# Kernel optimization log

Hardware: AMD Instinct MI355X
Metric: run time of the kernel (lower is better)

## Reference

```python
import jax, jax.numpy as jnp
import numpy as np

# ---- static physical configuration (matches init_kwargs param dict) ----
NX = NY = 513
NL = 3
N_ENS = 4
LX = LY = 5120.0e3
DX = LX / (NX - 1)
DY = LY / (NY - 1)
F0 = 9.375e-5
BETA = 1.754e-11
A2 = 0.0
A4 = 2.0e9
DELTA_EK = 2.0
TAU0 = 2.0e-5
BCCO = 0.2
ZFBC = BCCO / (1.0 + 0.5 * BCCO)
DT = 600.0
NUM_STEPS = 4
HEIGHTS = np.array([350.0, 750.0, 2900.0])
RED_G = np.array([0.025, 0.0125])

JAC_COEF = 1.0 / (F0 * DX * DY)
HYPERDIFF_COEF = A4 / F0**2 / DX**6
BOTTOM_FRICTION_COEF = DELTA_EK / (2.0 * abs(F0) * DX**2 * (-HEIGHTS[-1]))


def _build_constants():
    """Precompute stratification / mode / Helmholtz matrices (float64 numpy, cast to f32)."""
    A = np.zeros((NL, NL))
    A[0, 0] = 1.0 / (HEIGHTS[0] * RED_G[0])
    A[0, 1] = -1.0 / (HEIGHTS[0] * RED_G[0])
    for i in range(1, NL - 1):
        A[i, i - 1] = -1.0 / (HEIGHTS[i] * RED_G[i - 1])
        A[i, i] = 1.0 / HEIGHTS[i] * (1.0 / RED_G[i] + 1.0 / RED_G[i - 1])
        A[i, i + 1] = -1.0 / (HEIGHTS[i] * RED_G[i])
    A[-1, -1] = 1.0 / (HEIGHTS[NL - 1] * RED_G[NL - 2])
    A[-1, -2] = -1.0 / (HEIGHTS[NL - 1] * RED_G[NL - 2])
    lam_r, R = np.linalg.eig(A)
    lam_l, L = np.linalg.eig(A.T)
    lam_r, R, lam_l, L = lam_r.real, R.real, lam_l.real, L.real
    # align left eigenvectors with right eigenvalue ordering (biorthogonality)
    order = np.array([int(np.argmin(np.abs(lam_l - lr))) for lr in lam_r])
    L = L[:, order]
    Cl2m = np.diag(1.0 / np.diag(L.T @ R)) @ L.T
    Cm2l = R
    lambd = lam_r
    # DST-I eigenvalues of the 5-point Laplacian on the interior grid
    xg, yg = np.meshgrid(np.arange(1, NX - 1), np.arange(1, NY - 1), indexing='ij')
    lap_dst = (2 * (np.cos(np.pi / (NX - 1) * xg) - 1) / DX**2
               + 2 * (np.cos(np.pi / (NY - 1) * yg) - 1) / DY**2)
    helm_dst = lap_dst[None] / F0**2 - lambd[:, None, None]  # (nl, nx-2, ny-2)

    def np_dstI1D(x):
        N = x.shape[-1]
        xp = np.zeros(x.shape[:-1] + (N + 2,))
        xp[..., 1:-1] = x
        return np.fft.irfft(-1j * xp, n=2 * (N + 1), axis=-1, norm='ortho')[..., 1:N + 1]

    def np_dstI2D(x):
        return np.swapaxes(np_dstI1D(np.swapaxes(np_dstI1D(x), -1, -2)), -1, -2)

    const = np.ones((NL, NX, NY)) / (NX * NY)
    s = np.zeros_like(const)
    s[:, 1:-1, 1:-1] = np_dstI2D(np_dstI2D(const[:, 1:-1, 1:-1]) / helm_dst)
    hom_sol = (const + s * lambd[:, None, None])[:-1]  # (nl-1, nx, ny)
    M = (Cm2l[1:] - Cm2l[:-1])[:NL - 1, :NL - 1] * hom_sol.mean((1, 2))[None, :]
    alpha = -np.linalg.inv(M) @ (Cm2l[1:, :-1] - Cm2l[:-1, :-1])
    # wind forcing: curl(tau)/(f0*H1) on interior points; tau_y = 0, tau_x(y) only
    tau_x = -TAU0 * np.cos(2 * np.pi * (np.arange(NY) + 0.5) / NY)[None, :] * np.ones((NX, NY))
    dtaux_dy = (tau_x[1:-1, 2:] - tau_x[1:-1, :-2]) / (2 * DY)
    wind = (-dtaux_dy / (F0 * HEIGHTS[0]))[None]  # (1, nx-2, ny-2)
    f32 = lambda a: jnp.asarray(a, jnp.float32)
    return dict(A=f32(A), Cl2m=f32(Cl2m), Cm2l=f32(Cm2l), helmoltz_dst=f32(helm_dst),
                alpha_matrix=f32(alpha), homogeneous_sol=f32(hom_sol), wind_forcing=f32(wind))


# ---------------- stencil ops ----------------

def _pad11(x):
    return jnp.pad(x, [(0, 0)] * (x.ndim - 2) + [(1, 1), (1, 1)])


def laplacian_h_nobc(f):
    # unscaled 5-point Laplacian, interior values only: (..., nx-2, ny-2)
    return (f[..., 2:, 1:-1] + f[..., :-2, 1:-1] + f[..., 1:-1, 2:] + f[..., 1:-1, :-2]
            - 4.0 * f[..., 1:-1, 1:-1])


def laplacian_h(f, fc):
    # full-grid Laplacian with partial-slip boundary treatment (coefficient fc = zfbc)
    lap = _pad11(laplacian_h_nobc(f))
    lap = lap.at[..., 0, :].set(fc * (f[..., 1, :] - f[..., 0, :]))
    lap = lap.at[..., -1, :].set(fc * (f[..., -2, :] - f[..., -1, :]))
    lap = lap.at[..., :, 0].set(fc * (f[..., :, 1] - f[..., :, 0]))
    lap = lap.at[..., :, -1].set(fc * (f[..., :, -2] - f[..., :, -1]))
    return lap


def laplacian_h_boundaries(f, fc):
    # boundary Laplacian values, concat order: x=0 (y interior), x=-1, y=0 (full x), y=-1
    return jnp.concatenate([
        fc * (f[..., 1, 1:-1] - f[..., 0, 1:-1]),
        fc * (f[..., -2, 1:-1] - f[..., -1, 1:-1]),
        fc * (f[..., :, 1] - f[..., :, 0]),
        fc * (f[..., :, -2] - f[..., :, -1])], axis=-1)


def jacobi_h(f, g):
    # Arakawa 9-point Jacobian J(f, g), interior values (..., nx-2, ny-2)
    dx_f = f[..., 2:, :] - f[..., :-2, :]
    dx_g = g[..., 2:, :] - g[..., :-2, :]
    dy_f = f[..., 2:] - f[..., :-2]
    dy_g = g[..., 2:] - g[..., :-2]
    return ((dx_f[..., 1:-1] * dy_g[..., 1:-1, :] - dx_g[..., 1:-1] * dy_f[..., 1:-1, :])
            + (f[..., 2:, 1:-1] * dy_g[..., 2:, :] - f[..., :-2, 1:-1] * dy_g[..., :-2, :])
            - (f[..., 1:-1, 2:] * dx_g[..., 2:] - f[..., 1:-1, :-2] * dx_g[..., :-2])
            + (g[..., 1:-1, 2:] * dx_f[..., 2:] - g[..., 1:-1, :-2] * dx_f[..., :-2])
            - (g[..., 2:, 1:-1] * dy_f[..., 2:, :] - g[..., :-2, 1:-1] * dy_f[..., :-2, :])) / 12.0


# ---------------- DST-I elliptic solve ----------------

def dstI1D(x):
    N = x.shape[-1]
    z = jnp.zeros(x.shape[:-1] + (1,), x.dtype)
    xp = jnp.concatenate([z, x, z], axis=-1)
    return jnp.fft.irfft(-1j * xp.astype(jnp.complex64), n=2 * (N + 1), axis=-1,
                         norm='ortho')[..., 1:N + 1]


def dstI2D(x):
    return jnp.swapaxes(dstI1D(jnp.swapaxes(dstI1D(x), -1, -2)), -1, -2)


def inverse_elliptic_dst(f, op_dst):
    return dstI2D(dstI2D(f) / op_dst)


# ---------------- QG time derivative ----------------

def _time_derivatives(y, A, Cl2m, Cm2l, helm_dst, alpha, hom_sol, wind):
    q, p = y[0], y[1]  # (..., nl, nx, ny)
    # advection + hyperdiffusion RHS on interior (a_2 == 0 branch skipped as in source)
    rhs = JAC_COEF * jacobi_h(q, p)
    delta2_p = laplacian_h(p, ZFBC)
    rhs = rhs - HYPERDIFF_COEF * laplacian_h_nobc(laplacian_h(delta2_p, ZFBC))
    rhs = rhs.at[..., 0:1, :, :].add(wind)
    rhs = rhs.at[..., -1:, :, :].add(BOTTOM_FRICTION_COEF * laplacian_h_nobc(p[..., -1:, :, :]))
    dq = _pad11(rhs)
    # layers -> modes, DST Helmholtz inversion, homogeneous-solution correction
    rhs_h = jnp.einsum('ij,...jxy->...ixy', Cl2m, dq)
    dp_modes = _pad11(inverse_elliptic_dst(rhs_h[..., 1:-1, 1:-1], helm_dst))
    mean_m = dp_modes[..., :-1, :, :].mean((-2, -1))  # (..., nl-1)
    dalpha = jnp.einsum('ij,...j->...i', alpha, mean_m)[..., None, None]
    dp_modes = dp_modes.at[..., :-1, :, :].add(dalpha * hom_sol)
    dp = jnp.einsum('ij,...jxy->...ixy', Cm2l, dp_modes)
    # boundary vorticity update
    dp_bound = jnp.concatenate([dp[..., 0, 1:-1], dp[..., -1, 1:-1],
                                dp[..., :, 0], dp[..., :, -1]], axis=-1)
    delta_p_bound = laplacian_h_boundaries(dp / (F0 * DX)**2, ZFBC)
    dq_bound = delta_p_bound - jnp.einsum('ij,...jl->...il', A, dp_bound)
    ny2 = NY - 2
    dq = dq.at[..., 0, 1:-1].set(dq_bound[..., :ny2])
    dq = dq.at[..., -1, 1:-1].set(dq_bound[..., ny2:2 * ny2])
    dq = dq.at[..., :, 0].set(dq_bound[..., 2 * ny2:2 * ny2 + NX])
    dq = dq.at[..., :, -1].set(dq_bound[..., 2 * ny2 + NX:2 * ny2 + 2 * NX])
    return jnp.stack((dq, dp), 0)


def _forecast(y0, t, A, Cl2m, Cm2l, helm_dst, alpha, hom_sol, wind):
    deriv = lambda y: _time_derivatives(y, A, Cl2m, Cm2l, helm_dst, alpha, hom_sol, wind)

    def step(y, dt_):
        k1 = deriv(y)
        k2 = deriv(y + 0.5 * dt_ * k1)
        k3 = deriv(y + 0.5 * dt_ * k2)
        k4 = deriv(y + dt_ * k3)
        y_next = y + (dt_ / 6.0) * (k1 + 2.0 * k2 + 2.0 * k3 + k4)
        return y_next, y_next

    _, traj = jax.lax.scan(step, y0, t[1:] - t[:-1])
    return jnp.concatenate([y0[None], traj], axis=0)  # (T, 2, n_ens, nl, nx, ny)


def setup_inputs() -> dict:
    key = jax.random.key(0)
    y0 = 0.1 * jax.random.normal(key, (2, N_ENS, NL, NX, NY), dtype=jnp.float32)
    t = jnp.arange(NUM_STEPS + 1, dtype=jnp.float32) * DT
    consts = _build_constants()
    return dict(y0=y0, t=t, **consts)


def reference(y0, t, A, Cl2m, Cm2l, helmoltz_dst, alpha_matrix, homogeneous_sol, wind_forcing):
    return _forecast(y0, t, A, Cl2m, Cm2l, helmoltz_dst, alpha_matrix,
                     homogeneous_sol, wind_forcing)
```

## Files before the change

kernel.cpp:

```cpp
#include <hip/hip_runtime.h>
#include <math.h>

#define NXY 513
#define NIN 511
#define NL3 3
#define NE4 4
#define NB 12
#define GLD 512

static constexpr long FS  = (long)NE4 * NL3 * NXY * NXY;
static constexpr long GSZ = (long)NB * GLD * GLD;
static constexpr int  NSTEPS = 4;

static constexpr double dF0 = 9.375e-05;
static constexpr double dDX = 10000.0;
static constexpr float ZFBCf     = (float)(0.2 / (1.0 + 0.5 * 0.2));
static constexpr float JACCf     = (float)(1.0 / (dF0 * dDX * dDX));
static constexpr float HYPCf     = (float)(2.0e9 / (dF0 * dF0) / (dDX*dDX*dDX*dDX*dDX*dDX));
static constexpr float BFCf      = (float)(2.0 / (2.0 * dF0 * dDX * dDX * (-2900.0)));
static constexpr float INVF0DX2f = (float)(1.0 / ((dF0 * dDX) * (dF0 * dDX)));

typedef short  bf16x8 __attribute__((ext_vector_type(8)));
typedef float  f32x4  __attribute__((ext_vector_type(4)));
typedef unsigned int u32;
typedef __attribute__((address_space(1))) const u32 GAS;
typedef __attribute__((address_space(3))) u32 LAS;
#define GLDS(gp, lp) __builtin_amdgcn_global_load_lds((GAS*)(gp), (LAS*)(lp), 16, 0, 0)

__device__ __forceinline__ unsigned short f2bf(float x) {
    unsigned int u = __float_as_uint(x);
    return (unsigned short)((u + 0x7FFFu + ((u >> 16) & 1u)) >> 16);
}
__device__ __forceinline__ float bf2f(unsigned short h) {
    return __uint_as_float(((unsigned int)h) << 16);
}

__global__ void initB_kernel(unsigned short* __restrict__ BoH, unsigned short* __restrict__ BoL,
                             unsigned short* __restrict__ BeH, unsigned short* __restrict__ BeL) {
    int j = threadIdx.x;
    int n = blockIdx.x;
    int idx = n * 256 + j;
    int mo = ((n + 1) * (2 * j + 1)) & 1023;
    int me = ((n + 1) * (2 * j + 2)) & 1023;
    float fo = (float)(0.0625 * sin(M_PI * (double)mo / 512.0));
    float fe = (float)(0.0625 * sin(M_PI * (double)me / 512.0));
    unsigned short oh = f2bf(fo);
    BoH[idx] = oh; BoL[idx] = f2bf(fo - bf2f(oh));
    unsigned short eh = f2bf(fe);
    BeH[idx] = eh; BeL[idx] = f2bf(fe - bf2f(eh));
}

__global__ __launch_bounds__(256) void fused_rhs(
    float* __restrict__ kq, const float* __restrict__ q, const float* __restrict__ p,
    const float* __restrict__ wind)
{
    __shared__ float ps[22][72];
    __shared__ float qs[22][72];
    __shared__ float l1[22][72];
    __shared__ float l2[22][72];
    const int c  = blockIdx.z;
    const int x0 = 1 + blockIdx.y * 16;
    const int y0 = 1 + blockIdx.x * 64;
    const int t  = threadIdx.x;
    const size_t off = (size_t)c * NXY * NXY;
    const float* pp = p + off;
    const float* qp = q + off;

    for (int idx = t; idx < 22 * 70; idx += 256) {
        int i = idx / 70, j = idx % 70;
        int gx = x0 - 3 + i, gy = y0 - 3 + j;
        bool in = (gx >= 0 && gx < NXY && gy >= 0 && gy < NXY);
        size_t go = (size_t)gx * NXY + gy;
        ps[i][j] = in ? pp[go] : 0.f;
        qs[i][j] = in ? qp[go] : 0.f;
    }
    __syncthreads();

#define LAPBC(a, i, j, gx, gy) \
    ((gy) == 0       ? ZFBCf * (a[i][(j)+1] - a[i][j]) : \
     (gy) == NXY-1   ? ZFBCf * (a[i][(j)-1] - a[i][j]) : \
     (gx) == 0       ? ZFBCf * (a[(i)+1][j] - a[i][j]) : \
     (gx) == NXY-1   ? ZFBCf * (a[(i)-1][j] - a[i][j]) : \
     a[(i)+1][j] + a[(i)-1][j] + a[i][(j)+1] + a[i][(j)-1] - 4.f * a[i][j])

    for (int idx = t; idx < 20 * 68; idx += 256) {
        int i = 1 + idx / 68, j = 1 + idx % 68;
        int gx = x0 - 3 + i, gy = y0 - 3 + j;
        float v = 0.f;
        if (gx >= 0 && gx < NXY && gy >= 0 && gy < NXY) v = LAPBC(ps, i, j, gx, gy);
        l1[i][j] = v;
    }
    __syncthreads();

    for (int idx = t; idx < 18 * 66; idx += 256) {
        int i = 2 + idx / 66, j = 2 + idx % 66;
        int gx = x0 - 3 + i, gy = y0 - 3 + j;
        float v = 0.f;
        if (gx >= 0 && gx < NXY && gy >= 0 && gy < NXY) v = LAPBC(l1, i, j, gx, gy);
        l2[i][j] = v;
    }
    __syncthreads();
#undef LAPBC

    const int l = c % NL3;
    for (int idx = t; idx < 16 * 64; idx += 256) {
        int i = 3 + idx / 64, j = 3 + idx % 64;
        int gx = x0 - 3 + i, gy = y0 - 3 + j;
        if (gx > NIN || gy > NIN) continue;
        float fmm=qs[i-1][j-1], fm0=qs[i-1][j], fmp=qs[i-1][j+1];
        float f0m=qs[i][j-1],                    f0p=qs[i][j+1];
        float fpm=qs[i+1][j-1], fp0=qs[i+1][j], fpp=qs[i+1][j+1];
        float gmm=ps[i-1][j-1], gm0=ps[i-1][j], gmp=ps[i-1][j+1];
        float g0m=ps[i][j-1],   g00=ps[i][j],   g0p=ps[i][j+1];
        float gpm=ps[i+1][j-1], gp0=ps[i+1][j], gpp=ps[i+1][j+1];
        float J1 = (fp0 - fm0) * (g0p - g0m) - (gp0 - gm0) * (f0p - f0m);
        float J2 = fp0 * (gpp - gpm) - fm0 * (gmp - gmm);
        float J3 = f0p * (gpp - gmp) - f0m * (gpm - gmm);
        float J4 = g0p * (fpp - fmp) - g0m * (fpm - fmm);
        float J5 = gp0 * (fpp - fpm) - gm0 * (fmp - fmm);
        float jac = (J1 + J2 - J3 + J4 - J5) * (1.0f / 12.0f);
        float lap3 = l2[i+1][j] + l2[i-1][j] + l2[i][j+1] + l2[i][j-1] - 4.f * l2[i][j];
        float v = JACCf * jac - HYPCf * lap3;
        if (l == 0)       v += wind[(size_t)(gx-1) * NIN + (gy-1)];
        if (l == NL3-1)   v += BFCf * (gp0 + gm0 + g0p + g0m - 4.f * g00);
        kq[off + (size_t)gx * NXY + gy] = v;
    }
}

__global__ void l2m_kernel(unsigned short* __restrict__ Gh, unsigned short* __restrict__ Gl,
                           const float* __restrict__ kq, const float* __restrict__ Cl2m) {
    int p  = blockIdx.x * blockDim.x + threadIdx.x;
    int rx = blockIdx.y * blockDim.y + threadIdx.y;
    int e = blockIdx.z;
    int ry0 = 2 * p, ry1 = 2 * p + 1;
    float vA[3] = {0.f, 0.f, 0.f}, vB[3] = {0.f, 0.f, 0.f};
    if (rx < NIN) {
        size_t base = ((size_t)(e * NL3) * NXY + (rx + 1)) * NXY;
        if (ry0 < NIN) {
            float f0 = kq[base + ry0 + 1];
            float f1 = kq[base + (size_t)NXY*NXY + ry0 + 1];
            float f2 = kq[base + 2*(size_t)NXY*NXY + ry0 + 1];
            vA[0] = Cl2m[0]*f0 + Cl2m[1]*f1 + Cl2m[2]*f2;
            vA[1] = Cl2m[3]*f0 + Cl2m[4]*f1 + Cl2m[5]*f2;
            vA[2] = Cl2m[6]*f0 + Cl2m[7]*f1 + Cl2m[8]*f2;
        }
        if (ry1 < NIN) {
            float f0 = kq[base + ry1 + 1];
            float f1 = kq[base + (size_t)NXY*NXY + ry1 + 1];
            float f2 = kq[base + 2*(size_t)NXY*NXY + ry1 + 1];
            vB[0] = Cl2m[0]*f0 + Cl2m[1]*f1 + Cl2m[2]*f2;
            vB[1] = Cl2m[3]*f0 + Cl2m[4]*f1 + Cl2m[5]*f2;
            vB[2] = Cl2m[6]*f0 + Cl2m[7]*f1 + Cl2m[8]*f2;
        }
    }
#pragma unroll
    for (int i = 0; i < 3; ++i) {
        size_t pb = (size_t)(e * NL3 + i) * 262144;
        size_t po = pb + (size_t)rx * 256 + p;
        size_t pe = po + 131072;
        unsigned short ha = f2bf(vA[i]);
        Gh[po] = ha; Gl[po] = f2bf(vA[i] - bf2f(ha));
        unsigned short hb = f2bf(vB[i]);
        Gh[pe] = hb; Gl[pe] = f2bf(vB[i] - bf2f(hb));
    }
}

#define EPLD 68
__global__ __launch_bounds__(256, 3) void gemm_dst(
    const unsigned short* __restrict__ Ah, const unsigned short* __restrict__ Al,
    const unsigned short* __restrict__ BoH, const unsigned short* __restrict__ BoL,
    const unsigned short* __restrict__ BeH, const unsigned short* __restrict__ BeL,
    unsigned short* __restrict__ Ch, unsigned short* __restrict__ Cl,
    float* __restrict__ Cf, const float* __restrict__ helm, float* __restrict__ part)
{
    __shared__ __attribute__((aligned(16))) char lds[49152];
    __shared__ float red[256];
    float* ep1 = (float*)lds;
    float* ep2 = ep1 + 32 * EPLD;
    const int id = blockIdx.x;
    const int nblk = id / 96, rr = id - nblk * 96;
    const int b = rr >> 3, mblk = rr & 7;
    const int m0 = mblk << 6;
    const int n0t = nblk << 5;
    const int t = threadIdx.x;
    const int w = t >> 6, lane = t & 63;
    const int wn = w >> 1, wm = w & 1;
    const int lr = lane & 15, g = lane >> 4;
    const unsigned short* AbH = Ah + (size_t)b * 262144;
    const unsigned short* AbL = Al + (size_t)b * 262144;

    const int srA = t >> 2;
    const int scA = ((t & 3) ^ ((srA >> 1) & 3)) * 8;
    const size_t gA = (size_t)(m0 + srA) * 256 + scA;
    const int dA = t * 16;
    const int hid = t & 127;
    const int srB = hid >> 2;
    const int scB = ((hid & 3) ^ ((srB >> 1) & 3)) * 8;
    const size_t gB = (size_t)(n0t + srB) * 256 + scB;
    const unsigned short* B1 = (t < 128) ? BoH : BoL;
    const unsigned short* B2 = (t < 128) ? BeH : BeL;
    const int dB1 = ((t < 128) ? 16384 : 18432) + hid * 16;
    const int dB2 = ((t < 128) ? 20480 : 22528) + hid * 16;

    auto STAGE = [&](int buf, int kt) {
        char* bb = lds + buf * 24576;
        int ke = kt * 32;
        GLDS(AbH + gA + ke,          bb + dA);
        GLDS(AbL + gA + ke,          bb + 4096  + dA);
        GLDS(AbH + 131072 + gA + ke, bb + 8192  + dA);
        GLDS(AbL + 131072 + gA + ke, bb + 12288 + dA);
        GLDS(B1 + gB + ke, bb + dB1);
        GLDS(B2 + gB + ke, bb + dB2);
    };

    f32x4 accO[2] = {}, accE[2] = {};
    int abyte[2];
#pragma unroll
    for (int i = 0; i < 2; ++i) {
        int ar = wm*32 + i*16 + lr;
        abyte[i] = ar*64 + ((g ^ ((ar >> 1) & 3)) * 16);
    }
    const int brl = wn*16 + lr;
    const int bby = brl*64 + ((g ^ ((brl >> 1) & 3)) * 16);

    STAGE(0, 0);
    __syncthreads();
    for (int it = 0; it < 8; ++it) {
        const int buf = it & 1;
        if (it < 7) STAGE(buf ^ 1, it + 1);
        const char* bb = lds + buf * 24576;
        bf16x8 boH = *(const bf16x8*)(bb + 16384 + bby);
        bf16x8 boL = *(const bf16x8*)(bb + 18432 + bby);
        bf16x8 beH = *(const bf16x8*)(bb + 20480 + bby);
        bf16x8 beL = *(const bf16x8*)(bb + 22528 + bby);
#pragma unroll
        for (int i = 0; i < 2; ++i) {
            bf16x8 aoH = *(const bf16x8*)(bb + abyte[i]);
            bf16x8 aoL = *(const bf16x8*)(bb + 4096  + abyte[i]);
            bf16x8 aeH = *(const bf16x8*)(bb + 8192  + abyte[i]);
            bf16x8 aeL = *(const bf16x8*)(bb + 12288 + abyte[i]);
            accO[i] = __builtin_amdgcn_mfma_f32_16x16x32_bf16(aoH, boH, accO[i], 0, 0, 0);
            accO[i] = __builtin_amdgcn_mfma_f32_16x16x32_bf16(aoH, boL, accO[i], 0, 0, 0);
            accO[i] = __builtin_amdgcn_mfma_f32_16x16x32_bf16(aoL, boH, accO[i], 0, 0, 0);
            accE[i] = __builtin_amdgcn_mfma_f32_16x16x32_bf16(aeH, beH, accE[i], 0, 0, 0);
            accE[i] = __builtin_amdgcn_mfma_f32_16x16x32_bf16(aeH, beL, accE[i], 0, 0, 0);
            accE[i] = __builtin_amdgcn_mfma_f32_16x16x32_bf16(aeL, beH, accE[i], 0, 0, 0);
        }
        __syncthreads();
    }

    const int mode = b % NL3;
    const float* hp = helm ? (helm + (size_t)mode * NIN * NIN) : nullptr;
    const int nl = wn*16 + lr;
    const int r1g = n0t + nl;
    const int r2g = 510 - n0t - nl;
#pragma unroll
    for (int i = 0; i < 2; ++i) {
        int ml = wm*32 + i*16 + 4*g;
#pragma unroll
        for (int r = 0; r < 4; ++r) {
            float o = accO[i][r], e = accE[i][r];
            float v1 = o + e, v2 = o - e;
            int mg = m0 + ml + r;
            if (hp && mg < NIN) {
                v1 /= hp[(size_t)r1g * NIN + mg];
                v2 /= hp[(size_t)r2g * NIN + mg];
            }
            ep1[nl*EPLD + ml + r] = v1;
            ep2[nl*EPLD + ml + r] = v2;
        }
    }
    __syncthreads();

    float lsum = 0.f;
    {
        const int row = t >> 3;
        const int cb = (t & 7) * 8;
        const int r1 = n0t + row;
        const int r2 = 510 - n0t - row;
        float v1[8], v2[8];
#pragma unroll
        for (int k = 0; k < 8; ++k) { v1[k] = ep1[row*EPLD + cb + k]; v2[k] = ep2[row*EPLD + cb + k]; }
        if (Cf) {
            size_t c1 = (size_t)b*262144 + (size_t)r1*512 + m0 + cb;
            size_t c2 = (size_t)b*262144 + (size_t)r2*512 + m0 + cb;
            f32x4 a0 = {v1[0], v1[1], v1[2], v1[3]};
            f32x4 a1 = {v1[4], v1[5], v1[6], v1[7]};
            f32x4 b0 = {v2[0], v2[1], v2[2], v2[3]};
            f32x4 b1 = {v2[4], v2[5], v2[6], v2[7]};
            *(f32x4*)(Cf + c1) = a0; *(f32x4*)(Cf + c1 + 4) = a1;
            *(f32x4*)(Cf + c2) = b0; *(f32x4*)(Cf + c2 + 4) = b1;
            if (nblk == 0 && t < 64) Cf[(size_t)b*262144 + (size_t)511*512 + m0 + t] = 0.f;
#pragma unroll
            for (int k = 0; k < 8; ++k) lsum += v1[k];
            if (r1 != 255) {
#pragma unroll
                for (int k = 0; k < 8; ++k) lsum += v2[k];
            }
        } else {
            auto STROW = [&](int rrow, const float* v) {
                size_t po = (size_t)b*262144 + (size_t)rrow*256 + ((m0 + cb) >> 1);
                size_t pe = po + 131072;
                unsigned short eh[4], el[4], oh[4], ol[4];
#pragma unroll
                for (int k = 0; k < 4; ++k) {
                    float ve = v[2*k], vo = v[2*k+1];
                    eh[k] = f2bf(ve); el[k] = f2bf(ve - bf2f(eh[k]));
                    oh[k] = f2bf(vo); ol[k] = f2bf(vo - bf2f(oh[k]));
                }
                *(uint2*)(Ch + po) = make_uint2((u32)eh[0] | ((u32)eh[1] << 16), (u32)eh[2] | ((u32)eh[3] << 16));
                *(uint2*)(Cl + po) = make_uint2((u32)el[0] | ((u32)el[1] << 16), (u32)el[2] | ((u32)el[3] << 16));
                *(uint2*)(Ch + pe) = make_uint2((u32)oh[0] | ((u32)oh[1] << 16), (u32)oh[2] | ((u32)oh[3] << 16));
                *(uint2*)(Cl + pe) = make_uint2((u32)ol[0] | ((u32)ol[1] << 16), (u32)ol[2] | ((u32)ol[3] << 16));
            };
            STROW(r1, v1);
            STROW(r2, v2);
            if (nblk == 0 && t < 32) {
                size_t z = (size_t)b*262144 + (size_t)511*256 + (m0 >> 1) + t;
                Ch[z] = 0; Cl[z] = 0; Ch[z + 131072] = 0; Cl[z + 131072] = 0;
            }
        }
    }

    if (part && Cf && mode < 2) {
        __syncthreads();
        red[t] = lsum;
        __syncthreads();
        for (int w2 = 128; w2 >= 1; w2 >>= 1) {
            if (t < w2) red[t] += red[t + w2];
            __syncthreads();
        }
        if (t == 0) {
            int plane8 = (b / NL3) * 2 + mode;
            part[plane8 * 64 + nblk * 8 + mblk] = red[0];
        }
    }
}

__global__ __launch_bounds__(256) void m2l_bound(
    float* __restrict__ kp, float* __restrict__ kq,
    const float* __restrict__ G, const float* __restrict__ hom,
    const float* __restrict__ Cm2l, const float* __restrict__ Amat,
    const float* __restrict__ alpha, const float* __restrict__ part)
{
    __shared__ float sp[128];
    __shared__ float sdal[2];
    const int yy = blockIdx.x * 64 + threadIdx.x;
    const int xx = blockIdx.y * 4 + threadIdx.y;
    const int e  = blockIdx.z;
    const int tt = threadIdx.y * 64 + threadIdx.x;

    if (tt < 128) sp[tt] = part[(e*2 + (tt >> 6))*64 + (tt & 63)];
    __syncthreads();
    if (tt == 0) {
        float s0 = 0.f, s1 = 0.f;
        for (int j = 0; j < 64; ++j) { s0 += sp[j]; s1 += sp[64 + j]; }
        const float inv = 1.0f / ((float)NXY * (float)NXY);
        float mm0 = s0 * inv, mm1 = s1 * inv;
        sdal[0] = alpha[0]*mm0 + alpha[1]*mm1;
        sdal[1] = alpha[2]*mm0 + alpha[3]*mm1;
    }
    __syncthreads();
    if (xx >= NXY || yy >= NXY) return;
    const float dal0 = sdal[0], dal1 = sdal[1];

    auto DP = [&](int px, int py, float* dp) {
        bool inter = (px >= 1 && px <= NIN && py >= 1 && py <= NIN);
        float mv0 = 0.f, mv1 = 0.f, mv2 = 0.f;
        if (inter) {
            size_t gb = (size_t)(e*NL3)*GLD*GLD + (size_t)(px-1)*GLD + (py-1);
            mv0 = G[gb]; mv1 = G[gb + (size_t)GLD*GLD]; mv2 = G[gb + 2*(size_t)GLD*GLD];
        }
        mv0 += dal0 * hom[(size_t)px*NXY + py];
        mv1 += dal1 * hom[(size_t)NXY*NXY + (size_t)px*NXY + py];
        dp[0] = Cm2l[0]*mv0 + Cm2l[1]*mv1 + Cm2l[2]*mv2;
        dp[1] = Cm2l[3]*mv0 + Cm2l[4]*mv1 + Cm2l[5]*mv2;
        dp[2] = Cm2l[6]*mv0 + Cm2l[7]*mv1 + Cm2l[8]*mv2;
    };

    float dp[3];
    DP(xx, yy, dp);
#pragma unroll
    for (int l = 0; l < 3; ++l)
        kp[((size_t)(e*NL3 + l)*NXY + xx)*NXY + yy] = dp[l];

    const bool bnd = (xx == 0 || xx == NXY-1 || yy == 0 || yy == NXY-1);
    if (bnd) {
        int xn, yn;
        if      (yy == 0)      { xn = xx;    yn = 1; }
        else if (yy == NXY-1)  { xn = xx;    yn = NXY-2; }
        else if (xx == 0)      { xn = 1;     yn = yy; }
        else                   { xn = NXY-2; yn = yy; }
        float dpn[3];
        DP(xn, yn, dpn);
#pragma unroll
        for (int l = 0; l < 3; ++l) {
            float lpb = ZFBCf * INVF0DX2f * (dpn[l] - dp[l]);
            kq[((size_t)(e*NL3 + l)*NXY + xx)*NXY + yy] =
                lpb - (Amat[l*3+0]*dp[0] + Amat[l*3+1]*dp[1] + Amat[l*3+2]*dp[2]);
        }
    }
}

__global__ void rk_fused(float4* __restrict__ o1, float4* __restrict__ o2,
                         const float4* __restrict__ x, const float4* __restrict__ k,
                         float c1, float c2, int accumulate,
                         const float* __restrict__ t, int s, long n4) {
    float dt = t[s+1] - t[s];
    float a1 = c1 * dt, a2 = c2 * dt;
    for (long i = (long)blockIdx.x * blockDim.x + threadIdx.x; i < n4;
         i += (long)gridDim.x * blockDim.x) {
        float4 kk = k[i], xx = x[i];
        float4 b0 = accumulate ? o1[i] : xx;
        o1[i] = make_float4(b0.x + a1*kk.x, b0.y + a1*kk.y, b0.z + a1*kk.z, b0.w + a1*kk.w);
        if (o2) o2[i] = make_float4(xx.x + a2*kk.x, xx.y + a2*kk.y, xx.z + a2*kk.z, xx.w + a2*kk.w);
    }
}

__global__ void copy_kernel(float4* __restrict__ out, const float4* __restrict__ in, long n4) {
    for (long i = (long)blockIdx.x * blockDim.x + threadIdx.x; i < n4;
         i += (long)gridDim.x * blockDim.x)
        out[i] = in[i];
}

extern "C" void kernel_launch(void* const* d_in, const int* in_sizes, int n_in,
                              void* d_out, int out_size, void* d_ws, size_t ws_size,
                              hipStream_t stream) {
    const float* y0    = (const float*)d_in[0];
    const float* tarr  = (const float*)d_in[1];
    const float* Amat  = (const float*)d_in[2];
    const float* Cl2m  = (const float*)d_in[3];
    const float* Cm2l  = (const float*)d_in[4];
    const float* helm  = (const float*)d_in[5];
    const float* alpha = (const float*)d_in[6];
    const float* hom   = (const float*)d_in[7];
    const float* wind  = (const float*)d_in[8];
    float* out = (float*)d_out;
    char* base = (char*)d_ws;

    unsigned short* BoH = (unsigned short*)base;
    unsigned short* BoL = BoH + 65536;
    unsigned short* BeH = BoL + 65536;
    unsigned short* BeL = BeH + 65536;
    float* ytmp = (float*)(base + 1024*1024);
    float* kbuf = ytmp + 2*FS;
    char*  REGb = (char*)(kbuf + 2*FS);
    unsigned short* P0h = (unsigned short*)REGb;
    unsigned short* P0l = P0h + GSZ;
    unsigned short* P1h = P0l + GSZ;
    unsigned short* P1l = P1h + GSZ;
    float* R4 = (float*)REGb;
    float* partial = (float*)(REGb + (size_t)2*FS*sizeof(float));

    const dim3 bSt(64, 4, 1);
    const dim3 gSt4((NXY + 63)/64, (NXY + 3)/4, NE4);
    const dim3 gL2M(4, 128, NE4);
    const dim3 gF(8, 32, NB);
    const dim3 gG(768, 1, 1);
    const long n4 = 2*FS/4;

    initB_kernel<<<256, 256, 0, stream>>>(BoH, BoL, BeH, BeL);
    copy_kernel<<<1024, 256, 0, stream>>>((float4*)out, (const float4*)y0, n4);

    auto deriv = [&](const float* y, float* k) {
        const float* q = y;  const float* p = y + FS;
        float* kq = k;       float* kp = k + FS;
        fused_rhs<<<gF, 256, 0, stream>>>(kq, q, p, wind);
        l2m_kernel<<<gL2M, bSt, 0, stream>>>(P0h, P0l, kq, Cl2m);
        gemm_dst<<<gG, 256, 0, stream>>>(P0h, P0l, BoH, BoL, BeH, BeL, P1h, P1l, nullptr, nullptr, nullptr);
        gemm_dst<<<gG, 256, 0, stream>>>(P1h, P1l, BoH, BoL, BeH, BeL, P0h, P0l, nullptr, helm, nullptr);
        gemm_dst<<<gG, 256, 0, stream>>>(P0h, P0l, BoH, BoL, BeH, BeL, P1h, P1l, nullptr, nullptr, nullptr);
        gemm_dst<<<gG, 256, 0, stream>>>(P1h, P1l, BoH, BoL, BeH, BeL, nullptr, nullptr, R4, nullptr, partial);
        m2l_bound<<<gSt4, bSt, 0, stream>>>(kp, kq, R4, hom, Cm2l, Amat, alpha, partial);
    };

    for (int s = 0; s < NSTEPS; ++s) {
        float* ycur  = out + (size_t)s * 2 * FS;
        float* ynext = out + (size_t)(s + 1) * 2 * FS;
        deriv(ycur, kbuf);
        rk_fused<<<1024, 256, 0, stream>>>((float4*)ynext, (float4*)ytmp, (const float4*)ycur,
                                           (const float4*)kbuf, 1.f/6.f, 0.5f, 0, tarr, s, n4);
        deriv(ytmp, kbuf);
        rk_fused<<<1024, 256, 0, stream>>>((float4*)ynext, (float4*)ytmp, (const float4*)ycur,
                                           (const float4*)kbuf, 2.f/6.f, 0.5f, 1, tarr, s, n4);
        deriv(ytmp, kbuf);
        rk_fused<<<1024, 256, 0, stream>>>((float4*)ynext, (float4*)ytmp, (const float4*)ycur,
                                           (const float4*)kbuf, 2.f/6.f, 1.0f, 1, tarr, s, n4);
        deriv(ytmp, kbuf);
        rk_fused<<<1024, 256, 0, stream>>>((float4*)ynext, nullptr, (const float4*)ycur,
                                           (const float4*)kbuf, 1.f/6.f, 0.f, 1, tarr, s, n4);
    }
}
```

Baseline: 2.008 ms.

## Fuse four DST GEMM passes into one persistent kernel with grid barriers

The four back-to-back gemm_dst launches per derivative evaluation are merged into a single gemm4_dst kernel. It loops over the four passes, ping-ponging between the P0 and P1 buffers, and separates passes with a software grid-wide atomic barrier. The barrier counter is zeroed in copy_kernel. The aim is to remove three kernel launches and their inter-kernel drain gaps per derivative. In exchange, it relies on all 768 blocks being co-resident (3 per CU under the launch bounds), or the barrier deadlocks, and it adds barrier spin and atomic latency between passes.

```diff
diff --git a/kernel.cpp b/kernel.cpp
--- a/kernel.cpp
+++ b/kernel.cpp
@@ -7,6 +7,7 @@
 #define NE4 4
 #define NB 12
 #define GLD 512
+#define NBLK 768
 
 static constexpr long FS  = (long)NE4 * NL3 * NXY * NXY;
 static constexpr long GSZ = (long)NB * GLD * GLD;
@@ -33,6 +34,24 @@
 }
 __device__ __forceinline__ float bf2f(unsigned short h) {
     return __uint_as_float(((unsigned int)h) << 16);
+}
+
+__device__ __forceinline__ void grid_barrier(unsigned int* bar) {
+    __syncthreads();
+    if (threadIdx.x == 0) {
+        __threadfence();
+        unsigned int gen = __hip_atomic_load(&bar[1], __ATOMIC_RELAXED, __HIP_MEMORY_SCOPE_AGENT);
+        unsigned int a = __hip_atomic_fetch_add(&bar[0], 1u, __ATOMIC_RELAXED, __HIP_MEMORY_SCOPE_AGENT);
+        if (a == NBLK - 1) {
+            __hip_atomic_store(&bar[0], 0u, __ATOMIC_RELAXED, __HIP_MEMORY_SCOPE_AGENT);
+            __hip_atomic_fetch_add(&bar[1], 1u, __ATOMIC_RELEASE, __HIP_MEMORY_SCOPE_AGENT);
+        } else {
+            while (__hip_atomic_load(&bar[1], __ATOMIC_RELAXED, __HIP_MEMORY_SCOPE_AGENT) == gen)
+                __builtin_amdgcn_s_sleep(8);
+        }
+        __threadfence();
+    }
+    __syncthreads();
 }
 
 __global__ void initB_kernel(unsigned short* __restrict__ BoH, unsigned short* __restrict__ BoL,
@@ -166,12 +185,13 @@
 }
 
 #define EPLD 68
-__global__ __launch_bounds__(256, 3) void gemm_dst(
-    const unsigned short* __restrict__ Ah, const unsigned short* __restrict__ Al,
+__global__ __launch_bounds__(256, 3) void gemm4_dst(
+    unsigned short* __restrict__ P0h, unsigned short* __restrict__ P0l,
+    unsigned short* __restrict__ P1h, unsigned short* __restrict__ P1l,
     const unsigned short* __restrict__ BoH, const unsigned short* __restrict__ BoL,
     const unsigned short* __restrict__ BeH, const unsigned short* __restrict__ BeL,
-    unsigned short* __restrict__ Ch, unsigned short* __restrict__ Cl,
-    float* __restrict__ Cf, const float* __restrict__ helm, float* __restrict__ part)
+    float* __restrict__ R4, const float* __restrict__ helm, float* __restrict__ partial,
+    unsigned int* __restrict__ bar)
 {
     __shared__ __attribute__((aligned(16))) char lds[49152];
     __shared__ float red[256];
@@ -186,8 +206,6 @@
     const int w = t >> 6, lane = t & 63;
     const int wn = w >> 1, wm = w & 1;
     const int lr = lane & 15, g = lane >> 4;
-    const unsigned short* AbH = Ah + (size_t)b * 262144;
-    const unsigned short* AbL = Al + (size_t)b * 262144;
 
     const int srA = t >> 2;
     const int scA = ((t & 3) ^ ((srA >> 1) & 3)) * 8;
@@ -202,18 +220,6 @@
     const int dB1 = ((t < 128) ? 16384 : 18432) + hid * 16;
     const int dB2 = ((t < 128) ? 20480 : 22528) + hid * 16;
 
-    auto STAGE = [&](int buf, int kt) {
-        char* bb = lds + buf * 24576;
-        int ke = kt * 32;
-        GLDS(AbH + gA + ke,          bb + dA);
-        GLDS(AbL + gA + ke,          bb + 4096  + dA);
-        GLDS(AbH + 131072 + gA + ke, bb + 8192  + dA);
-        GLDS(AbL + 131072 + gA + ke, bb + 12288 + dA);
-        GLDS(B1 + gB + ke, bb + dB1);
-        GLDS(B2 + gB + ke, bb + dB2);
-    };
-
-    f32x4 accO[2] = {}, accE[2] = {};
     int abyte[2];
 #pragma unroll
     for (int i = 0; i < 2; ++i) {
@@ -222,117 +228,141 @@
     }
     const int brl = wn*16 + lr;
     const int bby = brl*64 + ((g ^ ((brl >> 1) & 3)) * 16);
-
-    STAGE(0, 0);
-    __syncthreads();
-    for (int it = 0; it < 8; ++it) {
-        const int buf = it & 1;
-        if (it < 7) STAGE(buf ^ 1, it + 1);
-        const char* bb = lds + buf * 24576;
-        bf16x8 boH = *(const bf16x8*)(bb + 16384 + bby);
-        bf16x8 boL = *(const bf16x8*)(bb + 18432 + bby);
-        bf16x8 beH = *(const bf16x8*)(bb + 20480 + bby);
-        bf16x8 beL = *(const bf16x8*)(bb + 22528 + bby);
+    const int mode = b % NL3;
+
+    for (int pass = 0; pass < 4; ++pass) {
+        if (pass) grid_barrier(bar);
+        const unsigned short* Ah = (pass & 1) ? P1h : P0h;
+        const unsigned short* Al = (pass & 1) ? P1l : P0l;
+        unsigned short* Ch  = (pass & 1) ? P0h : P1h;
+        unsigned short* Cl_ = (pass & 1) ? P0l : P1l;
+        float* Cf = (pass == 3) ? R4 : nullptr;
+        const float* hp = (pass == 1) ? (helm + (size_t)mode * NIN * NIN) : nullptr;
+        float* part = (pass == 3) ? partial : nullptr;
+        const unsigned short* AbH = Ah + (size_t)b * 262144;
+        const unsigned short* AbL = Al + (size_t)b * 262144;
+
+        auto STAGE = [&](int buf, int kt) {
+            char* bb = lds + buf * 24576;
+            int ke = kt * 32;
+            GLDS(AbH + gA + ke,          bb + dA);
+            GLDS(AbL + gA + ke,          bb + 4096  + dA);
+            GLDS(AbH + 131072 + gA + ke, bb + 8192  + dA);
+            GLDS(AbL + 131072 + gA + ke, bb + 12288 + dA);
+            GLDS(B1 + gB + ke, bb + dB1);
+            GLDS(B2 + gB + ke, bb + dB2);
+        };
+
+        f32x4 accO[2] = {}, accE[2] = {};
+        STAGE(0, 0);
+        __syncthreads();
+        for (int it = 0; it < 8; ++it) {
+            const int buf = it & 1;
+            if (it < 7) STAGE(buf ^ 1, it + 1);
+            const char* bb = lds + buf * 24576;
+            bf16x8 boH = *(const bf16x8*)(bb + 16384 + bby);
+            bf16x8 boL = *(const bf16x8*)(bb + 18432 + bby);
+            bf16x8 beH = *(const bf16x8*)(bb + 20480 + bby);
+            bf16x8 beL = *(const bf16x8*)(bb + 22528 + bby);
+#pragma unroll
+            for (int i = 0; i < 2; ++i) {
+                bf16x8 aoH = *(const bf16x8*)(bb + abyte[i]);
+                bf16x8 aoL = *(const bf16x8*)(bb + 4096  + abyte[i]);
+                bf16x8 aeH = *(const bf16x8*)(bb + 8192  + abyte[i]);
+                bf16x8 aeL = *(const bf16x8*)(bb + 12288 + abyte[i]);
+                accO[i] = __builtin_amdgcn_mfma_f32_16x16x32_bf16(aoH, boH, accO[i], 0, 0, 0);
+                accO[i] = __builtin_amdgcn_mfma_f32_16x16x32_bf16(aoH, boL, accO[i], 0, 0, 0);
+                accO[i] = __builtin_amdgcn_mfma_f32_16x16x32_bf16(aoL, boH, accO[i], 0, 0, 0);
+                accE[i] = __builtin_amdgcn_mfma_f32_16x16x32_bf16(aeH, beH, accE[i], 0, 0, 0);
+                accE[i] = __builtin_amdgcn_mfma_f32_16x16x32_bf16(aeH, beL, accE[i], 0, 0, 0);
+                accE[i] = __builtin_amdgcn_mfma_f32_16x16x32_bf16(aeL, beH, accE[i], 0, 0, 0);
+            }
+            __syncthreads();
+        }
+
+        const int nl = wn*16 + lr;
+        const int r1g = n0t + nl;
+        const int r2g = 510 - n0t - nl;
 #pragma unroll
         for (int i = 0; i < 2; ++i) {
-            bf16x8 aoH = *(const bf16x8*)(bb + abyte[i]);
-            bf16x8 aoL = *(const bf16x8*)(bb + 4096  + abyte[i]);
-            bf16x8 aeH = *(const bf16x8*)(bb + 8192  + abyte[i]);
-            bf16x8 aeL = *(const bf16x8*)(bb + 12288 + abyte[i]);
-            accO[i] = __builtin_amdgcn_mfma_f32_16x16x32_bf16(aoH, boH, accO[i], 0, 0, 0);
-            accO[i] = __builtin_amdgcn_mfma_f32_16x16x32_bf16(aoH, boL, accO[i], 0, 0, 0);
-            accO[i] = __builtin_amdgcn_mfma_f32_16x16x32_bf16(aoL, boH, accO[i], 0, 0, 0);
-            accE[i] = __builtin_amdgcn_mfma_f32_16x16x32_bf16(aeH, beH, accE[i], 0, 0, 0);
-            accE[i] = __builtin_amdgcn_mfma_f32_16x16x32_bf16(aeH, beL, accE[i], 0, 0, 0);
-            accE[i] = __builtin_amdgcn_mfma_f32_16x16x32_bf16(aeL, beH, accE[i], 0, 0, 0);
+            int ml = wm*32 + i*16 + 4*g;
+#pragma unroll
+            for (int r = 0; r < 4; ++r) {
+                float o = accO[i][r], e = accE[i][r];
+                float v1 = o + e, v2 = o - e;
+                int mg = m0 + ml + r;
+                if (hp && mg < NIN) {
+                    v1 /= hp[(size_t)r1g * NIN + mg];
+                    v2 /= hp[(size_t)r2g * NIN + mg];
+                }
+                ep1[nl*EPLD + ml + r] = v1;
+                ep2[nl*EPLD + ml + r] = v2;
+            }
         }
         __syncthreads();
-    }
-
-    const int mode = b % NL3;
-    const float* hp = helm ? (helm + (size_t)mode * NIN * NIN) : nullptr;
-    const int nl = wn*16 + lr;
-    const int r1g = n0t + nl;
-    const int r2g = 510 - n0t - nl;
-#pragma unroll
-    for (int i = 0; i < 2; ++i) {
-        int ml = wm*32 + i*16 + 4*g;
-#pragma unroll
-        for (int r = 0; r < 4; ++r) {
-            float o = accO[i][r], e = accE[i][r];
-            float v1 = o + e, v2 = o - e;
-            int mg = m0 + ml + r;
-            if (hp && mg < NIN) {
-                v1 /= hp[(size_t)r1g * NIN + mg];
-                v2 /= hp[(size_t)r2g * NIN + mg];
+
+        float lsum = 0.f;
+        {
+            const int row = t >> 3;
+            const int cb = (t & 7) * 8;
+            const int r1 = n0t + row;
+            const int r2 = 510 - n0t - row;
+            float v1[8], v2[8];
+#pragma unroll
+            for (int k = 0; k < 8; ++k) { v1[k] = ep1[row*EPLD + cb + k]; v2[k] = ep2[row*EPLD + cb + k]; }
+            if (Cf) {
+                size_t c1 = (size_t)b*262144 + (size_t)r1*512 + m0 + cb;
+                size_t c2 = (size_t)b*262144 + (size_t)r2*512 + m0 + cb;
+                f32x4 a0 = {v1[0], v1[1], v1[2], v1[3]};
+                f32x4 a1 = {v1[4], v1[5], v1[6], v1[7]};
+                f32x4 b0 = {v2[0], v2[1], v2[2], v2[3]};
+                f32x4 b1 = {v2[4], v2[5], v2[6], v2[7]};
+                *(f32x4*)(Cf + c1) = a0; *(f32x4*)(Cf + c1 + 4) = a1;
+                *(f32x4*)(Cf + c2) = b0; *(f32x4*)(Cf + c2 + 4) = b1;
+                if (nblk == 0 && t < 64) Cf[(size_t)b*262144 + (size_t)511*512 + m0 + t] = 0.f;
+#pragma unroll
+                for (int k = 0; k < 8; ++k) lsum += v1[k];
+                if (r1 != 255) {
+#pragma unroll
+                    for (int k = 0; k < 8; ++k) lsum += v2[k];
+                }
+            } else {
+                auto STROW = [&](int rrow, const float* v) {
+                    size_t po = (size_t)b*262144 + (size_t)rrow*256 + ((m0 + cb) >> 1);
+                    size_t pe = po + 131072;
+                    unsigned short eh[4], el[4], oh[4], ol[4];
+#pragma unroll
+                    for (int k = 0; k < 4; ++k) {
+                        float ve = v[2*k], vo = v[2*k+1];
+                        eh[k] = f2bf(ve); el[k] = f2bf(ve - bf2f(eh[k]));
+                        oh[k] = f2bf(vo); ol[k] = f2bf(vo - bf2f(oh[k]));
+                    }
+                    *(uint2*)(Ch + po)  = make_uint2((u32)eh[0] | ((u32)eh[1] << 16), (u32)eh[2] | ((u32)eh[3] << 16));
+                    *(uint2*)(Cl_ + po) = make_uint2((u32)el[0] | ((u32)el[1] << 16), (u32)el[2] | ((u32)el[3] << 16));
+                    *(uint2*)(Ch + pe)  = make_uint2((u32)oh[0] | ((u32)oh[1] << 16), (u32)oh[2] | ((u32)oh[3] << 16));
+                    *(uint2*)(Cl_ + pe) = make_uint2((u32)ol[0] | ((u32)ol[1] << 16), (u32)ol[2] | ((u32)ol[3] << 16));
+                };
+                STROW(r1, v1);
+                STROW(r2, v2);
+                if (nblk == 0 && t < 32) {
+                    size_t z = (size_t)b*262144 + (size_t)511*256 + (m0 >> 1) + t;
+                    Ch[z] = 0; Cl_[z] = 0; Ch[z + 131072] = 0; Cl_[z + 131072] = 0;
+                }
             }
-            ep1[nl*EPLD + ml + r] = v1;
-            ep2[nl*EPLD + ml + r] = v2;
-        }
-    }
-    __syncthreads();
-
-    float lsum = 0.f;
-    {
-        const int row = t >> 3;
-        const int cb = (t & 7) * 8;
-        const int r1 = n0t + row;
-        const int r2 = 510 - n0t - row;
-        float v1[8], v2[8];
-#pragma unroll
-        for (int k = 0; k < 8; ++k) { v1[k] = ep1[row*EPLD + cb + k]; v2[k] = ep2[row*EPLD + cb + k]; }
-        if (Cf) {
-            size_t c1 = (size_t)b*262144 + (size_t)r1*512 + m0 + cb;
-            size_t c2 = (size_t)b*262144 + (size_t)r2*512 + m0 + cb;
-            f32x4 a0 = {v1[0], v1[1], v1[2], v1[3]};
-            f32x4 a1 = {v1[4], v1[5], v1[6], v1[7]};
-            f32x4 b0 = {v2[0], v2[1], v2[2], v2[3]};
-            f32x4 b1 = {v2[4], v2[5], v2[6], v2[7]};
-            *(f32x4*)(Cf + c1) = a0; *(f32x4*)(Cf + c1 + 4) = a1;
-            *(f32x4*)(Cf + c2) = b0; *(f32x4*)(Cf + c2 + 4) = b1;
-            if (nblk == 0 && t < 64) Cf[(size_t)b*262144 + (size_t)511*512 + m0 + t] = 0.f;
-#pragma unroll
-            for (int k = 0; k < 8; ++k) lsum += v1[k];
-            if (r1 != 255) {
-#pragma unroll
-                for (int k = 0; k < 8; ++k) lsum += v2[k];
+        }
+
+        if (part && mode < 2) {
+            __syncthreads();
+            red[t] = lsum;
+            __syncthreads();
+            for (int w2 = 128; w2 >= 1; w2 >>= 1) {
+                if (t < w2) red[t] += red[t + w2];
+                __syncthreads();
             }
-        } else {
-            auto STROW = [&](int rrow, const float* v) {
-                size_t po = (size_t)b*262144 + (size_t)rrow*256 + ((m0 + cb) >> 1);
-                size_t pe = po + 131072;
-                unsigned short eh[4], el[4], oh[4], ol[4];
-#pragma unroll
-                for (int k = 0; k < 4; ++k) {
-                    float ve = v[2*k], vo = v[2*k+1];
-                    eh[k] = f2bf(ve); el[k] = f2bf(ve - bf2f(eh[k]));
-                    oh[k] = f2bf(vo); ol[k] = f2bf(vo - bf2f(oh[k]));
-                }
-                *(uint2*)(Ch + po) = make_uint2((u32)eh[0] | ((u32)eh[1] << 16), (u32)eh[2] | ((u32)eh[3] << 16));
-                *(uint2*)(Cl + po) = make_uint2((u32)el[0] | ((u32)el[1] << 16), (u32)el[2] | ((u32)el[3] << 16));
-                *(uint2*)(Ch + pe) = make_uint2((u32)oh[0] | ((u32)oh[1] << 16), (u32)oh[2] | ((u32)oh[3] << 16));
-                *(uint2*)(Cl + pe) = make_uint2((u32)ol[0] | ((u32)ol[1] << 16), (u32)ol[2] | ((u32)ol[3] << 16));
-            };
-            STROW(r1, v1);
-            STROW(r2, v2);
-            if (nblk == 0 && t < 32) {
-                size_t z = (size_t)b*262144 + (size_t)511*256 + (m0 >> 1) + t;
-                Ch[z] = 0; Cl[z] = 0; Ch[z + 131072] = 0; Cl[z + 131072] = 0;
+            if (t == 0) {
+                int plane8 = (b / NL3) * 2 + mode;
+                part[plane8 * 64 + nblk * 8 + mblk] = red[0];
             }
-        }
-    }
-
-    if (part && Cf && mode < 2) {
-        __syncthreads();
-        red[t] = lsum;
-        __syncthreads();
-        for (int w2 = 128; w2 >= 1; w2 >>= 1) {
-            if (t < w2) red[t] += red[t + w2];
-            __syncthreads();
-        }
-        if (t == 0) {
-            int plane8 = (b / NL3) * 2 + mode;
-            part[plane8 * 64 + nblk * 8 + mblk] = red[0];
         }
     }
 }
@@ -417,7 +447,9 @@
     }
 }
 
-__global__ void copy_kernel(float4* __restrict__ out, const float4* __restrict__ in, long n4) {
+__global__ void copy_kernel(float4* __restrict__ out, const float4* __restrict__ in, long n4,
+                            unsigned int* __restrict__ bar) {
+    if (blockIdx.x == 0 && threadIdx.x < 16) bar[threadIdx.x] = 0u;
     for (long i = (long)blockIdx.x * blockDim.x + threadIdx.x; i < n4;
          i += (long)gridDim.x * blockDim.x)
         out[i] = in[i];
@@ -451,26 +483,24 @@
     unsigned short* P1l = P1h + GSZ;
     float* R4 = (float*)REGb;
     float* partial = (float*)(REGb + (size_t)2*FS*sizeof(float));
+    unsigned int* bar = (unsigned int*)(partial + 512);
 
     const dim3 bSt(64, 4, 1);
     const dim3 gSt4((NXY + 63)/64, (NXY + 3)/4, NE4);
     const dim3 gL2M(4, 128, NE4);
     const dim3 gF(8, 32, NB);
-    const dim3 gG(768, 1, 1);
     const long n4 = 2*FS/4;
 
     initB_kernel<<<256, 256, 0, stream>>>(BoH, BoL, BeH, BeL);
-    copy_kernel<<<1024, 256, 0, stream>>>((float4*)out, (const float4*)y0, n4);
+    copy_kernel<<<1024, 256, 0, stream>>>((float4*)out, (const float4*)y0, n4, bar);
 
     auto deriv = [&](const float* y, float* k) {
         const float* q = y;  const float* p = y + FS;
         float* kq = k;       float* kp = k + FS;
         fused_rhs<<<gF, 256, 0, stream>>>(kq, q, p, wind);
         l2m_kernel<<<gL2M, bSt, 0, stream>>>(P0h, P0l, kq, Cl2m);
-        gemm_dst<<<gG, 256, 0, stream>>>(P0h, P0l, BoH, BoL, BeH, BeL, P1h, P1l, nullptr, nullptr, nullptr);
-        gemm_dst<<<gG, 256, 0, stream>>>(P1h, P1l, BoH, BoL, BeH, BeL, P0h, P0l, nullptr, helm, nullptr);
-        gemm_dst<<<gG, 256, 0, stream>>>(P0h, P0l, BoH, BoL, BeH, BeL, P1h, P1l, nullptr, nullptr, nullptr);
-        gemm_dst<<<gG, 256, 0, stream>>>(P1h, P1l, BoH, BoL, BeH, BeL, nullptr, nullptr, R4, nullptr, partial);
+        gemm4_dst<<<NBLK, 256, 0, stream>>>(P0h, P0l, P1h, P1l, BoH, BoL, BeH, BeL,
+                                            R4, helm, partial, bar);
         m2l_bound<<<gSt4, bSt, 0, stream>>>(kp, kq, R4, hom, Cm2l, Amat, alpha, partial);
     };
 
```

After: 6.101 ms. +203.8%, slower.
